# Kernel tuning notes

Hardware: AMD Instinct MI355X
Metric: run time of the kernel (lower is better)

Reference implementation:

```python
import jax, jax.numpy as jnp
import numpy as np

B, NLOC, F, H = 16384, 12, 512, 256

def setup_inputs() -> dict:
    key = jax.random.key(0)
    ks = jax.random.split(key, 8)
    s = lambda n: 1.0 / np.sqrt(n)
    return {
        "global_feature": jax.random.normal(ks[0], (B, F), jnp.float32),
        "local_features": jax.random.normal(ks[1], (B, NLOC, F), jnp.float32),
        "Wq": jax.random.normal(ks[2], (F, H), jnp.float32) * s(F),
        "bq": jnp.zeros((H,), jnp.float32),
        "Wk": jax.random.normal(ks[3], (F, H), jnp.float32) * s(F),
        "bk": jnp.zeros((H,), jnp.float32),
        "Wv": jax.random.normal(ks[4], (F, H), jnp.float32) * s(F),
        "bv": jnp.zeros((H,), jnp.float32),
        "w_dr": jax.random.normal(ks[5], (NLOC,), jnp.float32) * s(NLOC),  # Linear(12,1) weight
        "b_dr": jnp.zeros((), jnp.float32),
        "Wf": jax.random.normal(ks[6], (2 * H, F), jnp.float32) * s(2 * H),
        "bf": jnp.zeros((F,), jnp.float32),
    }

def reference(global_feature, local_features, Wq, bq, Wk, bk, Wv, bv, w_dr, b_dr, Wf, bf):
    scale = 1.0 / jnp.sqrt(jnp.float32(H))
    # dimension_reduction over the 12 local tokens: Linear(12 -> 1)
    lf_mean = jnp.einsum('bkf,k->bf', local_features, w_dr) + b_dr  # [B, F]
    # --- local queries attend to the single global token ---
    gk = global_feature @ Wk + bk                       # [B, H]
    gv = global_feature @ Wv + bv                       # [B, H]
    lq = local_features @ Wq + bq                       # [B, 12, H]
    s1 = (jnp.einsum('bkh,bh->bk', lq, gk) * scale)[..., None]  # [B, 12, 1]
    a1 = jax.nn.softmax(s1, axis=-1)                    # softmax over length-1 key axis
    weighted_global = a1 * gv[:, None, :]               # [B, 12, H]
    # --- global query attends over the 12 local tokens ---
    gq = global_feature @ Wq + bq                       # [B, H]
    lk = local_features @ Wk + bk                       # [B, 12, H]
    lv = local_features @ Wv + bv                       # [B, 12, H]
    s2 = jnp.einsum('bh,bkh->bk', gq, lk) * scale       # [B, 12]
    a2 = jax.nn.softmax(s2, axis=-1)
    local_to_global = jnp.einsum('bk,bkh->bh', a2, lv)  # [B, H]
    # pool the 12-token axis of the weighted global feature
    wg_mean = jnp.einsum('bkh,k->bh', weighted_global, w_dr) + b_dr  # [B, H]
    combined = jnp.concatenate([local_to_global, wg_mean], axis=-1)  # [B, 2H]
    fused = jax.nn.relu(combined @ Wf + bf) + lf_mean + global_feature  # [B, F]
    return fused
```

## Files before the change

kernel.cpp:

```cpp
#include <hip/hip_runtime.h>

#define B_SZ 16384
#define NLOC 12
#define F_DIM 512
#define H_DIM 256

typedef float f4 __attribute__((ext_vector_type(4)));
typedef _Float16 half4 __attribute__((ext_vector_type(4)));
typedef _Float16 half8 __attribute__((ext_vector_type(8)));

#define OFF_W1   0ul
#define OFF_W2   (OFF_W1 + 512ul*512*2)
#define OFF_C1   (OFF_W2 + 512ul*1024*2)
#define OFF_CVEC (OFF_C1 + 2048ul)
#define OFF_T    (OFF_CVEC + 2048ul)
#define OFF_ACAT (OFF_T + 16384ul*512*2)
#define OFF_LFM  (OFF_ACAT + 16384ul*1024*2)

__global__ void __launch_bounds__(256) precompute_w(
    const float* __restrict__ Wq, const float* __restrict__ Wk,
    const float* __restrict__ Wv, const float* __restrict__ Wf,
    const float* __restrict__ wdr,
    _Float16* __restrict__ W1, _Float16* __restrict__ W2)
{
    __shared__ float X[16][260];
    __shared__ float Y[16][260];
    const int mode = blockIdx.z;
    const int f0 = blockIdx.x * 16;
    const int j0 = blockIdx.y * 16;
    const int t = threadIdx.x;

    {
        const int r = t >> 4, hb = (t & 15) * 16;
        const float* ysrc = ((mode == 0) ? Wq : Wv) + (j0 + r) * H_DIM + hb;
#pragma unroll
        for (int u = 0; u < 16; u += 4)
            *(f4*)&Y[r][hb + u] = *(const f4*)(ysrc + u);
        if (mode == 0) {
            const float* xsrc = Wk + (f0 + r) * H_DIM + hb;
#pragma unroll
            for (int u = 0; u < 16; u += 4)
                *(f4*)&X[r][hb + u] = *(const f4*)(xsrc + u);
        }
    }
    if (mode != 0) {
        const int h = t;
        const int hoff = (mode == 2) ? H_DIM : 0;
        const float* xsrc = Wf + (long)(h + hoff) * F_DIM + f0;
#pragma unroll
        for (int r = 0; r < 16; ++r) X[r][h] = xsrc[r];
    }
    __syncthreads();

    const int fy = t >> 4, jx = t & 15;
    float acc = 0.f;
#pragma unroll 8
    for (int h = 0; h < H_DIM; ++h) acc += X[fy][h] * Y[jx][h];
    if (mode == 2) {
        float S = 0.f;
#pragma unroll
        for (int k = 0; k < NLOC; ++k) S += wdr[k];
        acc *= S;
    }
    if (mode == 0) W1[(f0 + fy) * F_DIM + (j0 + jx)] = (_Float16)acc;
    else W2[(long)(f0 + fy) * 1024 + ((mode == 2) ? F_DIM : 0) + (j0 + jx)] = (_Float16)acc;
}

__global__ void __launch_bounds__(256) cvec_kernel(
    const float* __restrict__ Wk, const float* __restrict__ Wf,
    const float* __restrict__ bq, const float* __restrict__ bv,
    const float* __restrict__ wdr, const float* __restrict__ bdr,
    const float* __restrict__ bfv,
    float* __restrict__ c1, float* __restrict__ cvec)
{
    const int f = blockIdx.x * 256 + threadIdx.x;
    f4 a = {0.f, 0.f, 0.f, 0.f};
    const f4* wk4 = (const f4*)(Wk + (long)f * H_DIM);
    const f4* bq4 = (const f4*)bq;
#pragma unroll 4
    for (int h4 = 0; h4 < H_DIM / 4; ++h4) a += wk4[h4] * bq4[h4];
    c1[f] = a[0] + a[1] + a[2] + a[3];

    float s1 = 0.f, s2 = 0.f, s3 = 0.f;
#pragma unroll 4
    for (int h = 0; h < H_DIM; ++h) {
        float w1v = Wf[h * F_DIM + f];
        float w2v = Wf[(H_DIM + h) * F_DIM + f];
        float bvh = bv[h];
        s1 += bvh * w1v; s2 += bvh * w2v; s3 += w2v;
    }
    float S = 0.f;
#pragma unroll
    for (int k = 0; k < NLOC; ++k) S += wdr[k];
    cvec[f] = s1 + S * s2 + bdr[0] * s3 + bfv[f];
}

__global__ void __launch_bounds__(256) cvt_g(
    const float* __restrict__ g, _Float16* __restrict__ Acat)
{
    const long i = (long)blockIdx.x * 256 + threadIdx.x;
    const long row = i >> 6;
    const int c8 = (int)(i & 63) * 8;
    f4 v0 = *(const f4*)(g + row * F_DIM + c8);
    f4 v1 = *(const f4*)(g + row * F_DIM + c8 + 4);
    half8 h;
#pragma unroll
    for (int j = 0; j < 4; ++j) { h[j] = (_Float16)v0[j]; h[4 + j] = (_Float16)v1[j]; }
    *(half8*)(Acat + row * 1024 + F_DIM + c8) = h;
}

template<int EPI>
__global__ void __launch_bounds__(256) gemm_bt(
    const _Float16* __restrict__ A, long lda,
    const _Float16* __restrict__ Bt, int K,
    _Float16* __restrict__ outh, float* __restrict__ outf,
    const float* __restrict__ addvec,
    const float* __restrict__ lfm, const float* __restrict__ gfeat)
{
    __shared__ _Float16 As[64][40];
    __shared__ _Float16 Bs[64][40];
    const int tid = threadIdx.x;
    const int lane = tid & 63;
    const int wave = tid >> 6;
    const int wm = (wave & 1) * 32;
    const int wn = (wave >> 1) * 32;
    const long m0 = (long)blockIdx.x * 64;
    const int n0 = blockIdx.y * 64;
    const int quad = lane >> 4;
    const int l16 = lane & 15;
    const int sr = tid >> 2;
    const int sc = (tid & 3) * 8;

    f4 acc[2][2] = {{{0.f,0.f,0.f,0.f},{0.f,0.f,0.f,0.f}},
                    {{0.f,0.f,0.f,0.f},{0.f,0.f,0.f,0.f}}};

    const _Float16* Aptr = A + (m0 + sr) * lda + sc;
    const _Float16* Bptr = Bt + (long)(n0 + sr) * K + sc;

    for (int k0 = 0; k0 < K; k0 += 32) {
        uint4 av = *(const uint4*)(Aptr + k0);
        uint4 bv = *(const uint4*)(Bptr + k0);
        *(uint4*)(&As[sr][sc]) = av;
        *(uint4*)(&Bs[sr][sc]) = bv;
        __syncthreads();
        half8 a0 = *(const half8*)(&As[wm + l16][quad * 8]);
        half8 a1 = *(const half8*)(&As[wm + 16 + l16][quad * 8]);
        half8 b0 = *(const half8*)(&Bs[wn + l16][quad * 8]);
        half8 b1 = *(const half8*)(&Bs[wn + 16 + l16][quad * 8]);
        acc[0][0] = __builtin_amdgcn_mfma_f32_16x16x32_f16(a0, b0, acc[0][0], 0, 0, 0);
        acc[0][1] = __builtin_amdgcn_mfma_f32_16x16x32_f16(a0, b1, acc[0][1], 0, 0, 0);
        acc[1][0] = __builtin_amdgcn_mfma_f32_16x16x32_f16(a1, b0, acc[1][0], 0, 0, 0);
        acc[1][1] = __builtin_amdgcn_mfma_f32_16x16x32_f16(a1, b1, acc[1][1], 0, 0, 0);
        __syncthreads();
    }

#pragma unroll
    for (int mi = 0; mi < 2; ++mi)
#pragma unroll
        for (int ni = 0; ni < 2; ++ni) {
            const int col = n0 + wn + ni * 16 + l16;
            const float av = addvec[col];
#pragma unroll
            for (int i = 0; i < 4; ++i) {
                const long row = m0 + wm + mi * 16 + quad * 4 + i;
                float v = acc[mi][ni][i] + av;
                if constexpr (EPI == 0) {
                    outh[row * F_DIM + col] = (_Float16)v;
                } else {
                    v = fmaxf(v, 0.f) + lfm[row * F_DIM + col] + gfeat[row * F_DIM + col];
                    outf[row * F_DIM + col] = v;
                }
            }
        }
}

__global__ void __launch_bounds__(256) local_pass(
    const float* __restrict__ loc, const _Float16* __restrict__ tbuf,
    const float* __restrict__ wdr, const float* __restrict__ bdr,
    _Float16* __restrict__ Acat, float* __restrict__ lfm)
{
    const int wave = threadIdx.x >> 6;
    const int lane = threadIdx.x & 63;
    const long b = (long)blockIdx.x * 4 + wave;
    const int c0 = lane * 4;
    const int c1 = 256 + lane * 4;
    const float* lb = loc + b * (NLOC * F_DIM);

    f4 la[NLOC], lbv[NLOC];
#pragma unroll
    for (int k = 0; k < NLOC; ++k) {
        la[k]  = *(const f4*)(lb + k * F_DIM + c0);
        lbv[k] = *(const f4*)(lb + k * F_DIM + c1);
    }
    half4 ta = *(const half4*)(tbuf + b * F_DIM + c0);
    half4 tb = *(const half4*)(tbuf + b * F_DIM + c1);
    f4 taf = __builtin_convertvector(ta, f4);
    f4 tbf = __builtin_convertvector(tb, f4);

    float p[NLOC];
#pragma unroll
    for (int k = 0; k < NLOC; ++k) {
        f4 prod = la[k] * taf + lbv[k] * tbf;
        p[k] = prod[0] + prod[1] + prod[2] + prod[3];
    }
#pragma unroll
    for (int k = 0; k < NLOC; ++k) {
        float v = p[k];
        v += __shfl_xor(v, 1);
        v += __shfl_xor(v, 2);
        v += __shfl_xor(v, 4);
        v += __shfl_xor(v, 8);
        v += __shfl_xor(v, 16);
        v += __shfl_xor(v, 32);
        p[k] = v * 0.0625f;
    }
    float mx = p[0];
#pragma unroll
    for (int k = 1; k < NLOC; ++k) mx = fmaxf(mx, p[k]);
    float e[NLOC], s = 0.f;
#pragma unroll
    for (int k = 0; k < NLOC; ++k) { e[k] = expf(p[k] - mx); s += e[k]; }
    const float inv = 1.f / s;

    f4 pA = {0.f,0.f,0.f,0.f}, pB = {0.f,0.f,0.f,0.f};
    f4 fA = {0.f,0.f,0.f,0.f}, fB = {0.f,0.f,0.f,0.f};
#pragma unroll
    for (int k = 0; k < NLOC; ++k) {
        const float ak = e[k] * inv;
        const float wk = wdr[k];
        pA += ak * la[k]; pB += ak * lbv[k];
        fA += wk * la[k]; fB += wk * lbv[k];
    }
    const float bd = bdr[0];
    fA += bd; fB += bd;
    *(half4*)(Acat + b * 1024 + c0) = __builtin_convertvector(pA, half4);
    *(half4*)(Acat + b * 1024 + c1) = __builtin_convertvector(pB, half4);
    *(f4*)(lfm + b * F_DIM + c0) = fA;
    *(f4*)(lfm + b * F_DIM + c1) = fB;
}

extern "C" void kernel_launch(void* const* d_in, const int* in_sizes, int n_in,
                              void* d_out, int out_size, void* d_ws, size_t ws_size,
                              hipStream_t stream)
{
    (void)in_sizes; (void)n_in; (void)out_size; (void)ws_size;
    const float* gf  = (const float*)d_in[0];
    const float* loc = (const float*)d_in[1];
    const float* Wq  = (const float*)d_in[2];
    const float* bq  = (const float*)d_in[3];
    const float* Wk  = (const float*)d_in[4];
    const float* Wv  = (const float*)d_in[6];
    const float* bv  = (const float*)d_in[7];
    const float* wdr = (const float*)d_in[8];
    const float* bdr = (const float*)d_in[9];
    const float* Wf  = (const float*)d_in[10];
    const float* bfv = (const float*)d_in[11];
    float* out = (float*)d_out;

    char* ws = (char*)d_ws;
    _Float16* W1   = (_Float16*)(ws + OFF_W1);
    _Float16* W2   = (_Float16*)(ws + OFF_W2);
    float*    c1   = (float*)(ws + OFF_C1);
    float*    cvec = (float*)(ws + OFF_CVEC);
    _Float16* tbuf = (_Float16*)(ws + OFF_T);
    _Float16* Acat = (_Float16*)(ws + OFF_ACAT);
    float*    lfm  = (float*)(ws + OFF_LFM);

    precompute_w<<<dim3(32, 32, 3), 256, 0, stream>>>(Wq, Wk, Wv, Wf, wdr, W1, W2);
    cvec_kernel<<<2, 256, 0, stream>>>(Wk, Wf, bq, bv, wdr, bdr, bfv, c1, cvec);
    cvt_g<<<4096, 256, 0, stream>>>(gf, Acat);
    gemm_bt<0><<<dim3(256, 8), 256, 0, stream>>>(Acat + F_DIM, 1024, W1, 512,
                                                 tbuf, nullptr, c1, nullptr, nullptr);
    local_pass<<<4096, 256, 0, stream>>>(loc, tbuf, wdr, bdr, Acat, lfm);
    gemm_bt<1><<<dim3(256, 8), 256, 0, stream>>>(Acat, 1024, W2, 1024,
                                                 nullptr, out, cvec, lfm, gf);
}
```

Before: 714.7 us.

## Fuse global conversion, first GEMM and local attention pass into one kernel

The fp16 conversion of the global feature, the global-to-T projection GEMM and the local attention pass are merged into one kernel that keeps G and T rows in shared memory. This removes the separate T buffer round trip and extra launches. The residual (lf_mean plus global feature) is precomputed as a single fp16 base tensor, replacing two fp32 reads in the final GEMM epilogue. The final GEMM moves to a 64x128 tile and the weight precompute to 32x32 tiles with 2x2 register blocking. The trade-offs are extra fp16 rounding in the residual path and only 512 blocks in the fused kernel, each holding about 75 KB of shared memory, which may limit occupancy.

```diff
diff --git a/kernel.cpp b/kernel.cpp
--- a/kernel.cpp
+++ b/kernel.cpp
@@ -1,6 +1,5 @@
 #include <hip/hip_runtime.h>
 
-#define B_SZ 16384
 #define NLOC 12
 #define F_DIM 512
 #define H_DIM 256
@@ -13,9 +12,8 @@
 #define OFF_W2   (OFF_W1 + 512ul*512*2)
 #define OFF_C1   (OFF_W2 + 512ul*1024*2)
 #define OFF_CVEC (OFF_C1 + 2048ul)
-#define OFF_T    (OFF_CVEC + 2048ul)
-#define OFF_ACAT (OFF_T + 16384ul*512*2)
-#define OFF_LFM  (OFF_ACAT + 16384ul*1024*2)
+#define OFF_ACAT (OFF_CVEC + 2048ul)
+#define OFF_BASE (OFF_ACAT + 16384ul*1024*2)
 
 __global__ void __launch_bounds__(256) precompute_w(
     const float* __restrict__ Wq, const float* __restrict__ Wk,
@@ -23,47 +21,64 @@
     const float* __restrict__ wdr,
     _Float16* __restrict__ W1, _Float16* __restrict__ W2)
 {
-    __shared__ float X[16][260];
-    __shared__ float Y[16][260];
+    __shared__ float X[32][264];
+    __shared__ float Y[32][264];
     const int mode = blockIdx.z;
-    const int f0 = blockIdx.x * 16;
-    const int j0 = blockIdx.y * 16;
+    const int f0 = blockIdx.x * 32;
+    const int j0 = blockIdx.y * 32;
     const int t = threadIdx.x;
 
     {
-        const int r = t >> 4, hb = (t & 15) * 16;
-        const float* ysrc = ((mode == 0) ? Wq : Wv) + (j0 + r) * H_DIM + hb;
-#pragma unroll
-        for (int u = 0; u < 16; u += 4)
-            *(f4*)&Y[r][hb + u] = *(const f4*)(ysrc + u);
+        const int r = t >> 3, cb = (t & 7) * 32;
+        const float* ysrc = ((mode == 0) ? Wq : Wv) + (j0 + r) * H_DIM + cb;
+#pragma unroll
+        for (int u = 0; u < 32; u += 4)
+            *(f4*)&Y[r][cb + u] = *(const f4*)(ysrc + u);
         if (mode == 0) {
-            const float* xsrc = Wk + (f0 + r) * H_DIM + hb;
-#pragma unroll
-            for (int u = 0; u < 16; u += 4)
-                *(f4*)&X[r][hb + u] = *(const f4*)(xsrc + u);
+            const float* xsrc = Wk + (f0 + r) * H_DIM + cb;
+#pragma unroll
+            for (int u = 0; u < 32; u += 4)
+                *(f4*)&X[r][cb + u] = *(const f4*)(xsrc + u);
         }
     }
     if (mode != 0) {
         const int h = t;
         const int hoff = (mode == 2) ? H_DIM : 0;
         const float* xsrc = Wf + (long)(h + hoff) * F_DIM + f0;
-#pragma unroll
-        for (int r = 0; r < 16; ++r) X[r][h] = xsrc[r];
+        f4 v[8];
+#pragma unroll
+        for (int u = 0; u < 8; ++u) v[u] = *(const f4*)(xsrc + u * 4);
+#pragma unroll
+        for (int r = 0; r < 32; ++r) X[r][h] = v[r >> 2][r & 3];
     }
     __syncthreads();
 
     const int fy = t >> 4, jx = t & 15;
-    float acc = 0.f;
+    float a00 = 0.f, a01 = 0.f, a10 = 0.f, a11 = 0.f;
 #pragma unroll 8
-    for (int h = 0; h < H_DIM; ++h) acc += X[fy][h] * Y[jx][h];
+    for (int h = 0; h < H_DIM; ++h) {
+        float x0 = X[fy][h], x1 = X[fy + 16][h];
+        float y0 = Y[jx][h], y1 = Y[jx + 16][h];
+        a00 += x0 * y0; a01 += x0 * y1; a10 += x1 * y0; a11 += x1 * y1;
+    }
     if (mode == 2) {
         float S = 0.f;
 #pragma unroll
         for (int k = 0; k < NLOC; ++k) S += wdr[k];
-        acc *= S;
-    }
-    if (mode == 0) W1[(f0 + fy) * F_DIM + (j0 + jx)] = (_Float16)acc;
-    else W2[(long)(f0 + fy) * 1024 + ((mode == 2) ? F_DIM : 0) + (j0 + jx)] = (_Float16)acc;
+        a00 *= S; a01 *= S; a10 *= S; a11 *= S;
+    }
+    if (mode == 0) {
+        W1[(f0 + fy) * F_DIM + (j0 + jx)]             = (_Float16)a00;
+        W1[(f0 + fy) * F_DIM + (j0 + jx + 16)]        = (_Float16)a01;
+        W1[(f0 + fy + 16) * F_DIM + (j0 + jx)]        = (_Float16)a10;
+        W1[(f0 + fy + 16) * F_DIM + (j0 + jx + 16)]   = (_Float16)a11;
+    } else {
+        const long co = (mode == 2) ? F_DIM : 0;
+        W2[(long)(f0 + fy) * 1024 + co + (j0 + jx)]           = (_Float16)a00;
+        W2[(long)(f0 + fy) * 1024 + co + (j0 + jx + 16)]      = (_Float16)a01;
+        W2[(long)(f0 + fy + 16) * 1024 + co + (j0 + jx)]      = (_Float16)a10;
+        W2[(long)(f0 + fy + 16) * 1024 + co + (j0 + jx + 16)] = (_Float16)a11;
+    }
 }
 
 __global__ void __launch_bounds__(256) cvec_kernel(
@@ -95,148 +110,205 @@
     cvec[f] = s1 + S * s2 + bdr[0] * s3 + bfv[f];
 }
 
-__global__ void __launch_bounds__(256) cvt_g(
-    const float* __restrict__ g, _Float16* __restrict__ Acat)
-{
-    const long i = (long)blockIdx.x * 256 + threadIdx.x;
-    const long row = i >> 6;
-    const int c8 = (int)(i & 63) * 8;
-    f4 v0 = *(const f4*)(g + row * F_DIM + c8);
-    f4 v1 = *(const f4*)(g + row * F_DIM + c8 + 4);
-    half8 h;
-#pragma unroll
-    for (int j = 0; j < 4; ++j) { h[j] = (_Float16)v0[j]; h[4 + j] = (_Float16)v1[j]; }
-    *(half8*)(Acat + row * 1024 + F_DIM + c8) = h;
-}
-
-template<int EPI>
-__global__ void __launch_bounds__(256) gemm_bt(
-    const _Float16* __restrict__ A, long lda,
-    const _Float16* __restrict__ Bt, int K,
-    _Float16* __restrict__ outh, float* __restrict__ outf,
-    const float* __restrict__ addvec,
-    const float* __restrict__ lfm, const float* __restrict__ gfeat)
-{
-    __shared__ _Float16 As[64][40];
-    __shared__ _Float16 Bs[64][40];
+__global__ void __launch_bounds__(256) fused_local(
+    const float* __restrict__ g, const float* __restrict__ loc,
+    const _Float16* __restrict__ W1, const float* __restrict__ c1,
+    const float* __restrict__ wdr, const float* __restrict__ bdr,
+    _Float16* __restrict__ Acat, _Float16* __restrict__ base)
+{
+    __shared__ _Float16 G[32][520];
+    __shared__ _Float16 T[32][520];
+    __shared__ _Float16 Bs[128][40];
     const int tid = threadIdx.x;
     const int lane = tid & 63;
     const int wave = tid >> 6;
-    const int wm = (wave & 1) * 32;
-    const int wn = (wave >> 1) * 32;
-    const long m0 = (long)blockIdx.x * 64;
-    const int n0 = blockIdx.y * 64;
     const int quad = lane >> 4;
     const int l16 = lane & 15;
-    const int sr = tid >> 2;
-    const int sc = (tid & 3) * 8;
-
-    f4 acc[2][2] = {{{0.f,0.f,0.f,0.f},{0.f,0.f,0.f,0.f}},
-                    {{0.f,0.f,0.f,0.f},{0.f,0.f,0.f,0.f}}};
-
-    const _Float16* Aptr = A + (m0 + sr) * lda + sc;
-    const _Float16* Bptr = Bt + (long)(n0 + sr) * K + sc;
-
-    for (int k0 = 0; k0 < K; k0 += 32) {
-        uint4 av = *(const uint4*)(Aptr + k0);
-        uint4 bv = *(const uint4*)(Bptr + k0);
-        *(uint4*)(&As[sr][sc]) = av;
-        *(uint4*)(&Bs[sr][sc]) = bv;
+    const long m0 = (long)blockIdx.x * 32;
+
+    {
+        const int r = tid >> 3;
+        const int cb = (tid & 7) * 8;
+#pragma unroll
+        for (int u = 0; u < 512; u += 64) {
+            const float* src = g + (m0 + r) * F_DIM + cb + u;
+            f4 v0 = *(const f4*)(src);
+            f4 v1 = *(const f4*)(src + 4);
+            half8 hv;
+#pragma unroll
+            for (int j = 0; j < 4; ++j) { hv[j] = (_Float16)v0[j]; hv[4 + j] = (_Float16)v1[j]; }
+            *(half8*)&G[r][cb + u] = hv;
+        }
+    }
+    __syncthreads();
+
+    const int srB = tid >> 1, scB = (tid & 1) * 16;
+    const int wn1 = wave * 32;
+    for (int nt = 0; nt < 4; ++nt) {
+        const int n0 = nt * 128;
+        f4 acc[2][2] = {{{0.f,0.f,0.f,0.f},{0.f,0.f,0.f,0.f}},
+                        {{0.f,0.f,0.f,0.f},{0.f,0.f,0.f,0.f}}};
+        for (int k0 = 0; k0 < 512; k0 += 32) {
+            const _Float16* wsrc = W1 + (n0 + srB) * F_DIM + k0 + scB;
+            uint4 w0 = *(const uint4*)(wsrc);
+            uint4 w1 = *(const uint4*)(wsrc + 8);
+            *(uint4*)&Bs[srB][scB] = w0;
+            *(uint4*)&Bs[srB][scB + 8] = w1;
+            __syncthreads();
+            half8 a0 = *(const half8*)&G[l16][k0 + quad * 8];
+            half8 a1 = *(const half8*)&G[16 + l16][k0 + quad * 8];
+            half8 b0 = *(const half8*)&Bs[wn1 + l16][quad * 8];
+            half8 b1 = *(const half8*)&Bs[wn1 + 16 + l16][quad * 8];
+            acc[0][0] = __builtin_amdgcn_mfma_f32_16x16x32_f16(a0, b0, acc[0][0], 0, 0, 0);
+            acc[0][1] = __builtin_amdgcn_mfma_f32_16x16x32_f16(a0, b1, acc[0][1], 0, 0, 0);
+            acc[1][0] = __builtin_amdgcn_mfma_f32_16x16x32_f16(a1, b0, acc[1][0], 0, 0, 0);
+            acc[1][1] = __builtin_amdgcn_mfma_f32_16x16x32_f16(a1, b1, acc[1][1], 0, 0, 0);
+            __syncthreads();
+        }
+#pragma unroll
+        for (int ni = 0; ni < 2; ++ni) {
+            const int col = n0 + wn1 + ni * 16 + l16;
+            const float cv = c1[col];
+#pragma unroll
+            for (int mi = 0; mi < 2; ++mi)
+#pragma unroll
+                for (int i = 0; i < 4; ++i)
+                    T[mi * 16 + quad * 4 + i][col] = (_Float16)(acc[mi][ni][i] + cv);
+        }
+    }
+    __syncthreads();
+
+    const int c0 = lane * 4;
+    const int c1i = 256 + lane * 4;
+    const float bd = bdr[0];
+    float wv[NLOC];
+#pragma unroll
+    for (int k = 0; k < NLOC; ++k) wv[k] = wdr[k];
+
+    for (int rr = 0; rr < 8; ++rr) {
+        const int bl = wave * 8 + rr;
+        const long b = m0 + bl;
+        const float* lb = loc + b * (NLOC * F_DIM);
+
+        f4 la[NLOC], lbv[NLOC];
+#pragma unroll
+        for (int k = 0; k < NLOC; ++k) {
+            la[k]  = *(const f4*)(lb + k * F_DIM + c0);
+            lbv[k] = *(const f4*)(lb + k * F_DIM + c1i);
+        }
+        f4 taf = __builtin_convertvector(*(const half4*)&T[bl][c0], f4);
+        f4 tbf = __builtin_convertvector(*(const half4*)&T[bl][c1i], f4);
+
+        float p[NLOC];
+#pragma unroll
+        for (int k = 0; k < NLOC; ++k) {
+            f4 prod = la[k] * taf + lbv[k] * tbf;
+            p[k] = prod[0] + prod[1] + prod[2] + prod[3];
+        }
+#pragma unroll
+        for (int k = 0; k < NLOC; ++k) {
+            float v = p[k];
+            v += __shfl_xor(v, 1);
+            v += __shfl_xor(v, 2);
+            v += __shfl_xor(v, 4);
+            v += __shfl_xor(v, 8);
+            v += __shfl_xor(v, 16);
+            v += __shfl_xor(v, 32);
+            p[k] = v * 0.0625f;
+        }
+        float mx = p[0];
+#pragma unroll
+        for (int k = 1; k < NLOC; ++k) mx = fmaxf(mx, p[k]);
+        float e[NLOC], s = 0.f;
+#pragma unroll
+        for (int k = 0; k < NLOC; ++k) { e[k] = expf(p[k] - mx); s += e[k]; }
+        const float inv = 1.f / s;
+
+        f4 pA = {0.f,0.f,0.f,0.f}, pB = {0.f,0.f,0.f,0.f};
+        f4 fA = {0.f,0.f,0.f,0.f}, fB = {0.f,0.f,0.f,0.f};
+#pragma unroll
+        for (int k = 0; k < NLOC; ++k) {
+            const float ak = e[k] * inv;
+            const float wk = wv[k];
+            pA += ak * la[k]; pB += ak * lbv[k];
+            fA += wk * la[k]; fB += wk * lbv[k];
+        }
+        half4 gA = *(const half4*)&G[bl][c0];
+        half4 gB = *(const half4*)&G[bl][c1i];
+        fA += bd + __builtin_convertvector(gA, f4);
+        fB += bd + __builtin_convertvector(gB, f4);
+
+        *(half4*)(Acat + b * 1024 + c0)          = __builtin_convertvector(pA, half4);
+        *(half4*)(Acat + b * 1024 + c1i)         = __builtin_convertvector(pB, half4);
+        *(half4*)(Acat + b * 1024 + 512 + c0)    = gA;
+        *(half4*)(Acat + b * 1024 + 512 + c1i)   = gB;
+        *(half4*)(base + b * F_DIM + c0)         = __builtin_convertvector(fA, half4);
+        *(half4*)(base + b * F_DIM + c1i)        = __builtin_convertvector(fB, half4);
+    }
+}
+
+__global__ void __launch_bounds__(256) gemm_final(
+    const _Float16* __restrict__ A, const _Float16* __restrict__ Bt,
+    const float* __restrict__ cvec, const _Float16* __restrict__ base,
+    float* __restrict__ out)
+{
+    __shared__ _Float16 As[64][40];
+    __shared__ _Float16 Bs[128][40];
+    const int tid = threadIdx.x;
+    const int lane = tid & 63;
+    const int wave = tid >> 6;
+    const int quad = lane >> 4;
+    const int l16 = lane & 15;
+    const int wm = (wave & 1) * 32;
+    const int wn = (wave >> 1) * 64;
+    const long m0 = (long)blockIdx.x * 64;
+    const int n0 = blockIdx.y * 128;
+    const int srA = tid >> 2, scA = (tid & 3) * 8;
+    const int srB = tid >> 1, scB = (tid & 1) * 16;
+
+    f4 acc[2][4];
+#pragma unroll
+    for (int mi = 0; mi < 2; ++mi)
+#pragma unroll
+        for (int nj = 0; nj < 4; ++nj) acc[mi][nj] = (f4){0.f,0.f,0.f,0.f};
+
+    for (int k0 = 0; k0 < 1024; k0 += 32) {
+        uint4 av = *(const uint4*)(A + (m0 + srA) * 1024 + k0 + scA);
+        const _Float16* bsrc = Bt + (long)(n0 + srB) * 1024 + k0 + scB;
+        uint4 b0v = *(const uint4*)(bsrc);
+        uint4 b1v = *(const uint4*)(bsrc + 8);
+        *(uint4*)&As[srA][scA] = av;
+        *(uint4*)&Bs[srB][scB] = b0v;
+        *(uint4*)&Bs[srB][scB + 8] = b1v;
         __syncthreads();
-        half8 a0 = *(const half8*)(&As[wm + l16][quad * 8]);
-        half8 a1 = *(const half8*)(&As[wm + 16 + l16][quad * 8]);
-        half8 b0 = *(const half8*)(&Bs[wn + l16][quad * 8]);
-        half8 b1 = *(const half8*)(&Bs[wn + 16 + l16][quad * 8]);
-        acc[0][0] = __builtin_amdgcn_mfma_f32_16x16x32_f16(a0, b0, acc[0][0], 0, 0, 0);
-        acc[0][1] = __builtin_amdgcn_mfma_f32_16x16x32_f16(a0, b1, acc[0][1], 0, 0, 0);
-        acc[1][0] = __builtin_amdgcn_mfma_f32_16x16x32_f16(a1, b0, acc[1][0], 0, 0, 0);
-        acc[1][1] = __builtin_amdgcn_mfma_f32_16x16x32_f16(a1, b1, acc[1][1], 0, 0, 0);
+        half8 a0 = *(const half8*)&As[wm + l16][quad * 8];
+        half8 a1 = *(const half8*)&As[wm + 16 + l16][quad * 8];
+        half8 bf[4];
+#pragma unroll
+        for (int nj = 0; nj < 4; ++nj)
+            bf[nj] = *(const half8*)&Bs[wn + nj * 16 + l16][quad * 8];
+#pragma unroll
+        for (int nj = 0; nj < 4; ++nj) {
+            acc[0][nj] = __builtin_amdgcn_mfma_f32_16x16x32_f16(a0, bf[nj], acc[0][nj], 0, 0, 0);
+            acc[1][nj] = __builtin_amdgcn_mfma_f32_16x16x32_f16(a1, bf[nj], acc[1][nj], 0, 0, 0);
+        }
         __syncthreads();
     }
 
 #pragma unroll
     for (int mi = 0; mi < 2; ++mi)
 #pragma unroll
-        for (int ni = 0; ni < 2; ++ni) {
-            const int col = n0 + wn + ni * 16 + l16;
-            const float av = addvec[col];
+        for (int nj = 0; nj < 4; ++nj) {
+            const int col = n0 + wn + nj * 16 + l16;
+            const float cv = cvec[col];
 #pragma unroll
             for (int i = 0; i < 4; ++i) {
                 const long row = m0 + wm + mi * 16 + quad * 4 + i;
-                float v = acc[mi][ni][i] + av;
-                if constexpr (EPI == 0) {
-                    outh[row * F_DIM + col] = (_Float16)v;
-                } else {
-                    v = fmaxf(v, 0.f) + lfm[row * F_DIM + col] + gfeat[row * F_DIM + col];
-                    outf[row * F_DIM + col] = v;
-                }
+                float v = acc[mi][nj][i] + cv;
+                v = fmaxf(v, 0.f) + (float)base[row * F_DIM + col];
+                out[row * F_DIM + col] = v;
             }
         }
-}
-
-__global__ void __launch_bounds__(256) local_pass(
-    const float* __restrict__ loc, const _Float16* __restrict__ tbuf,
-    const float* __restrict__ wdr, const float* __restrict__ bdr,
-    _Float16* __restrict__ Acat, float* __restrict__ lfm)
-{
-    const int wave = threadIdx.x >> 6;
-    const int lane = threadIdx.x & 63;
-    const long b = (long)blockIdx.x * 4 + wave;
-    const int c0 = lane * 4;
-    const int c1 = 256 + lane * 4;
-    const float* lb = loc + b * (NLOC * F_DIM);
-
-    f4 la[NLOC], lbv[NLOC];
-#pragma unroll
-    for (int k = 0; k < NLOC; ++k) {
-        la[k]  = *(const f4*)(lb + k * F_DIM + c0);
-        lbv[k] = *(const f4*)(lb + k * F_DIM + c1);
-    }
-    half4 ta = *(const half4*)(tbuf + b * F_DIM + c0);
-    half4 tb = *(const half4*)(tbuf + b * F_DIM + c1);
-    f4 taf = __builtin_convertvector(ta, f4);
-    f4 tbf = __builtin_convertvector(tb, f4);
-
-    float p[NLOC];
-#pragma unroll
-    for (int k = 0; k < NLOC; ++k) {
-        f4 prod = la[k] * taf + lbv[k] * tbf;
-        p[k] = prod[0] + prod[1] + prod[2] + prod[3];
-    }
-#pragma unroll
-    for (int k = 0; k < NLOC; ++k) {
-        float v = p[k];
-        v += __shfl_xor(v, 1);
-        v += __shfl_xor(v, 2);
-        v += __shfl_xor(v, 4);
-        v += __shfl_xor(v, 8);
-        v += __shfl_xor(v, 16);
-        v += __shfl_xor(v, 32);
-        p[k] = v * 0.0625f;
-    }
-    float mx = p[0];
-#pragma unroll
-    for (int k = 1; k < NLOC; ++k) mx = fmaxf(mx, p[k]);
-    float e[NLOC], s = 0.f;
-#pragma unroll
-    for (int k = 0; k < NLOC; ++k) { e[k] = expf(p[k] - mx); s += e[k]; }
-    const float inv = 1.f / s;
-
-    f4 pA = {0.f,0.f,0.f,0.f}, pB = {0.f,0.f,0.f,0.f};
-    f4 fA = {0.f,0.f,0.f,0.f}, fB = {0.f,0.f,0.f,0.f};
-#pragma unroll
-    for (int k = 0; k < NLOC; ++k) {
-        const float ak = e[k] * inv;
-        const float wk = wdr[k];
-        pA += ak * la[k]; pB += ak * lbv[k];
-        fA += wk * la[k]; fB += wk * lbv[k];
-    }
-    const float bd = bdr[0];
-    fA += bd; fB += bd;
-    *(half4*)(Acat + b * 1024 + c0) = __builtin_convertvector(pA, half4);
-    *(half4*)(Acat + b * 1024 + c1) = __builtin_convertvector(pB, half4);
-    *(f4*)(lfm + b * F_DIM + c0) = fA;
-    *(f4*)(lfm + b * F_DIM + c1) = fB;
 }
 
 extern "C" void kernel_launch(void* const* d_in, const int* in_sizes, int n_in,
@@ -262,16 +334,11 @@
     _Float16* W2   = (_Float16*)(ws + OFF_W2);
     float*    c1   = (float*)(ws + OFF_C1);
     float*    cvec = (float*)(ws + OFF_CVEC);
-    _Float16* tbuf = (_Float16*)(ws + OFF_T);
     _Float16* Acat = (_Float16*)(ws + OFF_ACAT);
-    float*    lfm  = (float*)(ws + OFF_LFM);
-
-    precompute_w<<<dim3(32, 32, 3), 256, 0, stream>>>(Wq, Wk, Wv, Wf, wdr, W1, W2);
+    _Float16* base = (_Float16*)(ws + OFF_BASE);
+
+    precompute_w<<<dim3(16, 16, 3), 256, 0, stream>>>(Wq, Wk, Wv, Wf, wdr, W1, W2);
     cvec_kernel<<<2, 256, 0, stream>>>(Wk, Wf, bq, bv, wdr, bdr, bfv, c1, cvec);
-    cvt_g<<<4096, 256, 0, stream>>>(gf, Acat);
-    gemm_bt<0><<<dim3(256, 8), 256, 0, stream>>>(Acat + F_DIM, 1024, W1, 512,
-                                                 tbuf, nullptr, c1, nullptr, nullptr);
-    local_pass<<<4096, 256, 0, stream>>>(loc, tbuf, wdr, bdr, Acat, lfm);
-    gemm_bt<1><<<dim3(256, 8), 256, 0, stream>>>(Acat, 1024, W2, 1024,
-                                                 nullptr, out, cvec, lfm, gf);
-}
+    fused_local<<<512, 256, 0, stream>>>(gf, loc, W1, c1, wdr, bdr, Acat, base);
+    gemm_final<<<dim3(256, 4), 256, 0, stream>>>(Acat, W2, cvec, base, out);
+}
```

Measured after the change: 710.4 us. No clear change (-0.6%).
